# Performance work log

Measured on AMD Instinct MI355X. Metric: run time of the kernel, lower is better.

Reference implementation:

```python
import jax, jax.numpy as jnp
import numpy as np

B, N, FEAT = 64, 1024, 3
HID, STATE, LAYERS, NTYPES = 64, 32, 2, 10


def setup_inputs() -> dict:
    key = jax.random.key(0)
    ks = jax.random.split(key, 16)
    s = 0.1
    return {
        "task_features": jax.random.normal(ks[0], (B, N, FEAT), jnp.float32),
        "task_types": jax.random.randint(ks[1], (B, N), 0, NTYPES, jnp.int32),
        "prev_state": jnp.zeros((B, STATE), jnp.float32),
        "enc_w1": jax.random.normal(ks[2], (HID, FEAT), jnp.float32) * s,
        "enc_b1": jnp.zeros((HID,), jnp.float32),
        "enc_w2": jax.random.normal(ks[3], (HID, HID), jnp.float32) * s,
        "enc_b2": jnp.zeros((HID,), jnp.float32),
        "contention": jax.random.normal(ks[4], (NTYPES, NTYPES), jnp.float32) * 0.1,
        "gnn_w": jax.random.normal(ks[5], (LAYERS, HID, HID), jnp.float32) * s,
        "gnn_b": jnp.zeros((LAYERS, HID), jnp.float32),
        "gru_w_ih": jax.random.normal(ks[6], (3 * STATE, HID), jnp.float32) * s,
        "gru_w_hh": jax.random.normal(ks[7], (3 * STATE, STATE), jnp.float32) * s,
        "gru_b_ih": jnp.zeros((3 * STATE,), jnp.float32),
        "gru_b_hh": jnp.zeros((3 * STATE,), jnp.float32),
        "head_w1": jax.random.normal(ks[8], (HID, HID + STATE), jnp.float32) * s,
        "head_b1": jnp.zeros((HID,), jnp.float32),
        "head_w2": jax.random.normal(ks[9], (1, HID), jnp.float32) * s,
        "head_b2": jnp.zeros((1,), jnp.float32),
    }


def _forward(task_features, task_types, prev_state, enc_w1, enc_b1, enc_w2, enc_b2,
             contention, gnn_w, gnn_b, gru_w_ih, gru_w_hh, gru_b_ih, gru_b_hh,
             head_w1, head_b1, head_w2, head_b2):
    # task encoder: Linear -> ReLU -> Linear
    emb = jax.nn.relu(task_features @ enc_w1.T + enc_b1) @ enc_w2.T + enc_b2  # (B,N,H)
    # interaction graph: type-pair gather + cosine similarity
    base = contention[task_types[:, :, None], task_types[:, None, :]]  # (B,N,N)
    nrm = emb / jnp.maximum(jnp.linalg.norm(emb, axis=-1, keepdims=True), 1e-12)
    sim = jnp.einsum("bnd,bmd->bnm", nrm, nrm)
    adjacency = jax.nn.sigmoid(base) * sim  # (B,N,N)
    # GNN layers: aggregate + linear + relu
    h = emb
    for l in range(LAYERS):
        agg = jnp.einsum("bnm,bmd->bnd", adjacency, h)
        h = jax.nn.relu((h + agg) @ gnn_w[l].T + gnn_b[l])
    ctx = h.mean(axis=1)  # (B,H)
    # GRUCell (torch semantics)
    gi = ctx @ gru_w_ih.T + gru_b_ih
    gh = prev_state @ gru_w_hh.T + gru_b_hh
    i_r, i_z, i_n = jnp.split(gi, 3, axis=-1)
    h_r, h_z, h_n = jnp.split(gh, 3, axis=-1)
    r = jax.nn.sigmoid(i_r + h_r)
    z = jax.nn.sigmoid(i_z + h_z)
    n = jnp.tanh(i_n + r * h_n)
    new_state = (1.0 - z) * n + z * prev_state  # (B,S)
    # latency head on [h, state]
    st = jnp.broadcast_to(new_state[:, None, :], (h.shape[0], h.shape[1], new_state.shape[-1]))
    combined = jnp.concatenate([h, st], axis=-1)
    lat = jax.nn.relu(combined @ head_w1.T + head_b1) @ head_w2.T + head_b2
    return lat[..., 0], new_state


def reference(task_features, task_types, prev_state, enc_w1, enc_b1, enc_w2, enc_b2,
              contention, gnn_w, gnn_b, gru_w_ih, gru_w_hh, gru_b_ih, gru_b_hh,
              head_w1, head_b1, head_w2, head_b2):
    return _forward(task_features, task_types, prev_state, enc_w1, enc_b1, enc_w2, enc_b2,
                    contention, gnn_w, gnn_b, gru_w_ih, gru_w_hh, gru_b_ih, gru_b_hh,
                    head_w1, head_b1, head_w2, head_b2)
```

## Files before the change

### kernel.cpp

```cpp
#include <hip/hip_runtime.h>
#include <math.h>

#define BB 64
#define NN 1024
#define HID 64
#define STATE 32
#define NTYPES 10

typedef _Float16 f16;
typedef f16 f16x8 __attribute__((ext_vector_type(8)));
typedef float f32x4 __attribute__((ext_vector_type(4)));

#define MFMA16(a, b, c) __builtin_amdgcn_mfma_f32_16x16x32_f16(a, b, c, 0, 0, 0)

__device__ __forceinline__ float sigm(float x) { return 1.f / (1.f + expf(-x)); }

__device__ __forceinline__ f16x8 cvt8(float4 a, float4 b) {
    f16x8 r;
    r[0] = (f16)a.x; r[1] = (f16)a.y; r[2] = (f16)a.z; r[3] = (f16)a.w;
    r[4] = (f16)b.x; r[5] = (f16)b.y; r[6] = (f16)b.z; r[7] = (f16)b.w;
    return r;
}

__global__ __launch_bounds__(256) void k_prep(
    const float* __restrict__ w2, const float* __restrict__ gw,
    const float* __restrict__ hw1, f16* __restrict__ out)
{
    int p = blockIdx.x * 256 + threadIdx.x;
    if (p >= 18432) return;
    const float* W; int K, pl;
    if (p < 12288) { int seg = p >> 12; pl = p & 4095; W = (seg == 0) ? w2 : gw + (seg - 1) * 4096; K = 64; }
    else { W = hw1; K = 96; pl = p - 12288; }
    int j = pl & 7, lane = (pl >> 3) & 63, nt = (pl >> 9) & 3, ch = pl >> 11;
    int k = ch * 32 + ((lane >> 4) << 3) + j;
    int o = nt * 16 + (lane & 15);
    out[p] = (f16)W[o * K + k];
}

__global__ __launch_bounds__(256) void k_encoder(
    const float* __restrict__ feat,
    const float* __restrict__ w1, const float* __restrict__ b1,
    const f16* __restrict__ w2f, const float* __restrict__ b2,
    float* __restrict__ emb, float* __restrict__ nrm)
{
    __shared__ f16 w2s[4096];
    __shared__ f16 tmp[4][16 * 72];
    __shared__ float fbuf[4][48];
    int tid = threadIdx.x, wave = tid >> 6, lane = tid & 63;
    int l15 = lane & 15, quad = lane >> 4;
    { const uint4* s = (const uint4*)w2f; uint4* d = (uint4*)w2s;
      for (int i = tid; i < 512; i += 256) d[i] = s[i]; }
    float w10 = w1[lane * 3], w11 = w1[lane * 3 + 1], w12 = w1[lane * 3 + 2], b1l = b1[lane];
    int tb = blockIdx.x * 64 + wave * 16;
    if (lane < 48) fbuf[wave][lane] = feat[tb * 3 + lane];
    __syncthreads();
    f16* tw = &tmp[wave][0];
#pragma unroll
    for (int r = 0; r < 16; ++r) {
        float x0 = fbuf[wave][r * 3], x1 = fbuf[wave][r * 3 + 1], x2 = fbuf[wave][r * 3 + 2];
        float hv = fmaxf(fmaf(w10, x0, fmaf(w11, x1, fmaf(w12, x2, b1l))), 0.f);
        tw[r * 72 + lane] = (f16)hv;
    }
    __builtin_amdgcn_sched_barrier(0);
    f16x8 a0 = *(const f16x8*)&tw[l15 * 72 + quad * 8];
    f16x8 a1 = *(const f16x8*)&tw[l15 * 72 + 32 + quad * 8];
    const f16x8* bf = (const f16x8*)w2s;
    f32x4 acc[4];
#pragma unroll
    for (int nt = 0; nt < 4; ++nt) {
        f32x4 c = {0.f, 0.f, 0.f, 0.f};
        c = MFMA16(a0, bf[(0 * 4 + nt) * 64 + lane], c);
        c = MFMA16(a1, bf[(1 * 4 + nt) * 64 + lane], c);
        acc[nt] = c;
    }
    float b2c[4];
#pragma unroll
    for (int nt = 0; nt < 4; ++nt) b2c[nt] = b2[nt * 16 + l15];
#pragma unroll
    for (int i = 0; i < 4; ++i) {
        float v[4]; float ss = 0.f;
#pragma unroll
        for (int nt = 0; nt < 4; ++nt) { v[nt] = acc[nt][i] + b2c[nt]; ss = fmaf(v[nt], v[nt], ss); }
        ss += __shfl_xor(ss, 1, 64); ss += __shfl_xor(ss, 2, 64);
        ss += __shfl_xor(ss, 4, 64); ss += __shfl_xor(ss, 8, 64);
        float rinv = 1.f / fmaxf(sqrtf(ss), 1e-12f);
        int grow = tb + quad * 4 + i;
#pragma unroll
        for (int nt = 0; nt < 4; ++nt) {
            emb[grow * 64 + nt * 16 + l15] = v[nt];
            nrm[grow * 64 + nt * 16 + l15] = v[nt] * rinv;
        }
    }
}

__global__ __launch_bounds__(256) void k_bucket(
    const int* __restrict__ types, int* __restrict__ idx, int* __restrict__ cnt,
    float* __restrict__ ctx)
{
    int b = blockIdx.x;
    __shared__ int lcnt[NTYPES];
    if (threadIdx.x < NTYPES) lcnt[threadIdx.x] = 0;
    if (threadIdx.x < HID) ctx[b * HID + threadIdx.x] = 0.f;
    __syncthreads();
    for (int m = threadIdx.x; m < NN; m += 256) {
        int t = types[b * NN + m];
        int pos = atomicAdd(&lcnt[t], 1);
        idx[(b * NTYPES + t) * NN + pos] = m;
    }
    __syncthreads();
    if (threadIdx.x < NTYPES) cnt[b * NTYPES + threadIdx.x] = lcnt[threadIdx.x];
}

__global__ __launch_bounds__(256) void k_buildM(
    const int* __restrict__ idx, const int* __restrict__ cnt,
    const float* __restrict__ nrm, const float* __restrict__ h,
    f16* __restrict__ M)
{
    int b = blockIdx.x / NTYPES, j = blockIdx.x % NTYPES;
    int c = cnt[b * NTYPES + j];
    const int* lst = idx + (b * NTYPES + j) * NN;
    int kq = threadIdx.x >> 4, dq = threadIdx.x & 15;
    float acc[4][4] = {};
    const float4* nrm4 = (const float4*)(nrm + (size_t)b * NN * HID);
    const float4* h4   = (const float4*)(h   + (size_t)b * NN * HID);
    int e = 0;
    for (; e + 8 <= c; e += 8) {
        int ms[8];
#pragma unroll
        for (int u = 0; u < 8; ++u) ms[u] = lst[e + u];
        float4 av4[8], hv4[8];
#pragma unroll
        for (int u = 0; u < 8; ++u) { av4[u] = nrm4[ms[u] * 16 + kq]; hv4[u] = h4[ms[u] * 16 + dq]; }
#pragma unroll
        for (int u = 0; u < 8; ++u) {
            float av[4] = {av4[u].x, av4[u].y, av4[u].z, av4[u].w};
            float hv[4] = {hv4[u].x, hv4[u].y, hv4[u].z, hv4[u].w};
#pragma unroll
            for (int i = 0; i < 4; ++i)
#pragma unroll
                for (int q = 0; q < 4; ++q)
                    acc[i][q] = fmaf(av[i], hv[q], acc[i][q]);
        }
    }
    for (; e < c; ++e) {
        int m = lst[e];
        float4 a = nrm4[m * 16 + kq];
        float4 hh = h4[m * 16 + dq];
        float av[4] = {a.x, a.y, a.z, a.w};
        float hv[4] = {hh.x, hh.y, hh.z, hh.w};
#pragma unroll
        for (int i = 0; i < 4; ++i)
#pragma unroll
            for (int q = 0; q < 4; ++q)
                acc[i][q] = fmaf(av[i], hv[q], acc[i][q]);
    }
    f16* Mo = M + ((size_t)(b * NTYPES + j)) * HID * HID;
#pragma unroll
    for (int i = 0; i < 4; ++i) {
        union { f16 h[4]; uint2 u; } pk;
#pragma unroll
        for (int q = 0; q < 4; ++q) pk.h[q] = (f16)acc[i][q];
        *(uint2*)&Mo[(kq * 4 + i) * 64 + dq * 4] = pk.u;
    }
}

__global__ __launch_bounds__(256) void k_gnn_layer(
    const int* __restrict__ idx, const int* __restrict__ cnt,
    const float* __restrict__ cont, const f16* __restrict__ M,
    const float* __restrict__ nrm, const float* __restrict__ h,
    const f16* __restrict__ gwf, const float* __restrict__ gb,
    float* __restrict__ hout, float* __restrict__ ctx)
{
    __shared__ f16 cs[4096];
    __shared__ f16 gs[4096];
    __shared__ f16 tmp[4][16 * 72];
    int b = blockIdx.x / NTYPES, t = blockIdx.x % NTYPES;
    int c = cnt[b * NTYPES + t];
    if (c == 0) return;
    int tid = threadIdx.x, wave = tid >> 6, lane = tid & 63;
    int l15 = lane & 15, quad = lane >> 4;
    { const uint4* s2 = (const uint4*)gwf; uint4* d2 = (uint4*)gs;
      for (int i = tid; i < 512; i += 256) d2[i] = s2[i]; }
    {
        float sg[NTYPES];
#pragma unroll
        for (int j = 0; j < NTYPES; ++j) sg[j] = sigm(cont[t * NTYPES + j]);
        const f16* Mb = M + (size_t)b * NTYPES * 4096;
        for (int p = tid; p < 4096; p += 256) {
            float a = 0.f;
#pragma unroll
            for (int j = 0; j < NTYPES; ++j) a = fmaf(sg[j], (float)Mb[j * 4096 + p], a);
            int k = p >> 6, n = p & 63;
            int pos = (((k >> 5) * 4 + (n >> 4)) * 64 + ((k >> 3) & 3) * 16 + (n & 15)) * 8 + (k & 7);
            cs[pos] = (f16)a;
        }
    }
    float gbl[4];
#pragma unroll
    for (int nt = 0; nt < 4; ++nt) gbl[nt] = gb[nt * 16 + l15];
    const int* lst = idx + (b * NTYPES + t) * NN;
    const float* nb = nrm + (size_t)b * NN * HID;
    const float* hb = h + (size_t)b * NN * HID;
    float* hob = hout + (size_t)b * NN * HID;
    __syncthreads();
    const f16x8* cbf = (const f16x8*)cs;
    const f16x8* gbf = (const f16x8*)gs;
    f16* tw = &tmp[wave][0];
    float cacc[4] = {0.f, 0.f, 0.f, 0.f};
    for (int tb = wave * 16; tb < c; tb += 64) {
        int rA = tb + l15; if (rA >= c) rA = c - 1;
        int mA = lst[rA];
        const float4* na = (const float4*)(nb + (size_t)mA * 64);
        f16x8 a0 = cvt8(na[quad * 2], na[quad * 2 + 1]);
        f16x8 a1 = cvt8(na[8 + quad * 2], na[8 + quad * 2 + 1]);
        int rS[4], mS[4]; float hl[4][4];
#pragma unroll
        for (int i = 0; i < 4; ++i) {
            rS[i] = tb + quad * 4 + i;
            int rc = rS[i] < c ? rS[i] : c - 1;
            mS[i] = lst[rc];
#pragma unroll
            for (int nt = 0; nt < 4; ++nt) hl[nt][i] = hb[(size_t)mS[i] * 64 + nt * 16 + l15];
        }
        f32x4 acc[4];
#pragma unroll
        for (int nt = 0; nt < 4; ++nt) {
            f32x4 cc = {0.f, 0.f, 0.f, 0.f};
            cc = MFMA16(a0, cbf[(0 * 4 + nt) * 64 + lane], cc);
            cc = MFMA16(a1, cbf[(1 * 4 + nt) * 64 + lane], cc);
            acc[nt] = cc;
        }
#pragma unroll
        for (int nt = 0; nt < 4; ++nt)
#pragma unroll
            for (int i = 0; i < 4; ++i)
                tw[(quad * 4 + i) * 72 + nt * 16 + l15] = (f16)(acc[nt][i] + hl[nt][i]);
        __builtin_amdgcn_sched_barrier(0);
        f16x8 t0 = *(const f16x8*)&tw[l15 * 72 + quad * 8];
        f16x8 t1 = *(const f16x8*)&tw[l15 * 72 + 32 + quad * 8];
#pragma unroll
        for (int nt = 0; nt < 4; ++nt) {
            f32x4 o = {0.f, 0.f, 0.f, 0.f};
            o = MFMA16(t0, gbf[(0 * 4 + nt) * 64 + lane], o);
            o = MFMA16(t1, gbf[(1 * 4 + nt) * 64 + lane], o);
#pragma unroll
            for (int i = 0; i < 4; ++i)
                if (rS[i] < c) {
                    float v = fmaxf(o[i] + gbl[nt], 0.f);
                    hob[(size_t)mS[i] * 64 + nt * 16 + l15] = v;
                    cacc[nt] += v;
                }
        }
        __builtin_amdgcn_sched_barrier(0);
    }
    if (ctx) {
#pragma unroll
        for (int nt = 0; nt < 4; ++nt) {
            float s = cacc[nt];
            s += __shfl_xor(s, 16, 64);
            s += __shfl_xor(s, 32, 64);
            if (quad == 0) atomicAdd(&ctx[b * HID + nt * 16 + l15], s);
        }
    }
}

__global__ __launch_bounds__(128) void k_gru(
    const float* __restrict__ ctx_sum, const float* __restrict__ prev,
    const float* __restrict__ w_ih, const float* __restrict__ w_hh,
    const float* __restrict__ b_ih, const float* __restrict__ b_hh,
    float* __restrict__ state_out)
{
    int b = blockIdx.x;
    int tid = threadIdx.x;
    __shared__ float cs[HID], ps[STATE], gis[96], ghs[96];
    if (tid < HID) cs[tid] = ctx_sum[b * HID + tid] * (1.f / NN);
    if (tid >= HID && tid < HID + STATE) ps[tid - HID] = prev[b * STATE + tid - HID];
    __syncthreads();
    if (tid < 96) {
        float gi = b_ih[tid];
#pragma unroll 8
        for (int k = 0; k < HID; ++k) gi = fmaf(w_ih[tid * HID + k], cs[k], gi);
        float gh = b_hh[tid];
#pragma unroll
        for (int k = 0; k < STATE; ++k) gh = fmaf(w_hh[tid * STATE + k], ps[k], gh);
        gis[tid] = gi; ghs[tid] = gh;
    }
    __syncthreads();
    if (tid < STATE) {
        float r = sigm(gis[tid] + ghs[tid]);
        float z = sigm(gis[32 + tid] + ghs[32 + tid]);
        float nn = tanhf(gis[64 + tid] + r * ghs[64 + tid]);
        float pv = ps[tid];
        state_out[b * STATE + tid] = (1.f - z) * nn + z * pv;
    }
}

__global__ __launch_bounds__(256) void k_head(
    const float* __restrict__ h2, const float* __restrict__ state,
    const f16* __restrict__ hwf, const float* __restrict__ b1,
    const float* __restrict__ w2, const float* __restrict__ b2,
    float* __restrict__ lat)
{
    __shared__ f16 ws_[6144];
    int tid = threadIdx.x, wave = tid >> 6, lane = tid & 63;
    int l15 = lane & 15, quad = lane >> 4;
    int b = blockIdx.x >> 4;
    { const uint4* s = (const uint4*)hwf; uint4* d = (uint4*)ws_;
      for (int i = tid; i < 768; i += 256) d[i] = s[i]; }
    float b1c[4], w2c[4];
#pragma unroll
    for (int nt = 0; nt < 4; ++nt) { b1c[nt] = b1[nt * 16 + l15]; w2c[nt] = w2[nt * 16 + l15]; }
    float b2v = b2[0];
    __syncthreads();
    int tb = blockIdx.x * 64 + wave * 16;
    int grow = tb + l15;
    const float4* ha = (const float4*)(h2 + (size_t)grow * 64);
    f16x8 a0 = cvt8(ha[quad * 2], ha[quad * 2 + 1]);
    f16x8 a1 = cvt8(ha[8 + quad * 2], ha[8 + quad * 2 + 1]);
    const float4* sp = (const float4*)(state + b * STATE);
    f16x8 a2 = cvt8(sp[quad * 2], sp[quad * 2 + 1]);
    const f16x8* bf = (const f16x8*)ws_;
    f32x4 acc[4];
#pragma unroll
    for (int nt = 0; nt < 4; ++nt) {
        f32x4 cc = {0.f, 0.f, 0.f, 0.f};
        cc = MFMA16(a0, bf[(0 * 4 + nt) * 64 + lane], cc);
        cc = MFMA16(a1, bf[(1 * 4 + nt) * 64 + lane], cc);
        cc = MFMA16(a2, bf[(2 * 4 + nt) * 64 + lane], cc);
        acc[nt] = cc;
    }
#pragma unroll
    for (int i = 0; i < 4; ++i) {
        float s = 0.f;
#pragma unroll
        for (int nt = 0; nt < 4; ++nt) s = fmaf(fmaxf(acc[nt][i] + b1c[nt], 0.f), w2c[nt], s);
        s += __shfl_xor(s, 1, 64); s += __shfl_xor(s, 2, 64);
        s += __shfl_xor(s, 4, 64); s += __shfl_xor(s, 8, 64);
        if (l15 == 0) lat[tb + quad * 4 + i] = s + b2v;
    }
}

extern "C" void kernel_launch(void* const* d_in, const int* in_sizes, int n_in,
                              void* d_out, int out_size, void* d_ws, size_t ws_size,
                              hipStream_t stream) {
    const float* feat   = (const float*)d_in[0];
    const int*   types  = (const int*)d_in[1];
    const float* prev   = (const float*)d_in[2];
    const float* enc_w1 = (const float*)d_in[3];
    const float* enc_b1 = (const float*)d_in[4];
    const float* enc_w2 = (const float*)d_in[5];
    const float* enc_b2 = (const float*)d_in[6];
    const float* cont   = (const float*)d_in[7];
    const float* gnn_w  = (const float*)d_in[8];
    const float* gnn_b  = (const float*)d_in[9];
    const float* w_ih   = (const float*)d_in[10];
    const float* w_hh   = (const float*)d_in[11];
    const float* b_ih   = (const float*)d_in[12];
    const float* b_hh   = (const float*)d_in[13];
    const float* hw1    = (const float*)d_in[14];
    const float* hb1    = (const float*)d_in[15];
    const float* hw2    = (const float*)d_in[16];
    const float* hb2    = (const float*)d_in[17];
    float* out = (float*)d_out;

    float* ws  = (float*)d_ws;
    float* h0  = ws;
    float* h1  = ws + 4194304;
    float* nrm = ws + 8388608;
    int*   idx = (int*)(ws + 12582912);
    int*   cnt = idx + BB * NTYPES * NN;
    f16*   M    = (f16*)(ws + 12582912 + 656000);
    f16*   wfrag = (f16*)(ws + 12582912 + 656000 + 1310720);
    float* ctx  = ws + 12582912 + 656000 + 1310720 + 9216;
    f16*   w2f  = wfrag;
    f16*   gw0f = wfrag + 4096;
    f16*   gw1f = wfrag + 8192;
    f16*   hwf  = wfrag + 12288;

    k_prep<<<72, 256, 0, stream>>>(enc_w2, gnn_w, hw1, wfrag);
    k_encoder<<<BB * NN / 64, 256, 0, stream>>>(feat, enc_w1, enc_b1, w2f, enc_b2, h0, nrm);
    k_bucket<<<BB, 256, 0, stream>>>(types, idx, cnt, ctx);
    k_buildM<<<BB * NTYPES, 256, 0, stream>>>(idx, cnt, nrm, h0, M);
    k_gnn_layer<<<BB * NTYPES, 256, 0, stream>>>(idx, cnt, cont, M, nrm, h0, gw0f, gnn_b, h1, nullptr);
    k_buildM<<<BB * NTYPES, 256, 0, stream>>>(idx, cnt, nrm, h1, M);
    k_gnn_layer<<<BB * NTYPES, 256, 0, stream>>>(idx, cnt, cont, M, nrm, h1, gw1f, gnn_b + HID, h0, ctx);
    k_gru<<<BB, 128, 0, stream>>>(ctx, prev, w_ih, w_hh, b_ih, b_hh, out + BB * NN);
    k_head<<<BB * NN / 64, 256, 0, stream>>>(h0, out + BB * NN, hwf, hb1, hw2, hb2, out);
}
```

Baseline: 204.8 us.

## Precompute C·W per type, split buildM and GNN over four blocks, fuse bucketing

Folds the GNN weight into the per-type aggregation matrix, so a new kernel computes D = C·W once per (batch, type). The layer kernel then does a single accumulated MFMA chain (nrm·D + h·W) and no longer runs a second MFMA pass through shared memory. buildM and the GNN layer are split across four blocks each to raise parallelism. Bucketing moves into the encoder using global atomics, and zeroing moves into the prep kernel. This drops one launch but adds the buildCD launches and makes index order nondeterministic.

```diff
diff --git a/kernel.cpp b/kernel.cpp
--- a/kernel.cpp
+++ b/kernel.cpp
@@ -22,25 +22,32 @@
     return r;
 }
 
-__global__ __launch_bounds__(256) void k_prep(
+__global__ __launch_bounds__(256) void k_misc(
     const float* __restrict__ w2, const float* __restrict__ gw,
-    const float* __restrict__ hw1, f16* __restrict__ out)
+    const float* __restrict__ hw1, f16* __restrict__ out,
+    int* __restrict__ cnt, float* __restrict__ ctx)
 {
     int p = blockIdx.x * 256 + threadIdx.x;
-    if (p >= 18432) return;
-    const float* W; int K, pl;
-    if (p < 12288) { int seg = p >> 12; pl = p & 4095; W = (seg == 0) ? w2 : gw + (seg - 1) * 4096; K = 64; }
-    else { W = hw1; K = 96; pl = p - 12288; }
-    int j = pl & 7, lane = (pl >> 3) & 63, nt = (pl >> 9) & 3, ch = pl >> 11;
-    int k = ch * 32 + ((lane >> 4) << 3) + j;
-    int o = nt * 16 + (lane & 15);
-    out[p] = (f16)W[o * K + k];
+    if (p < 18432) {
+        const float* W; int K, pl;
+        if (p < 12288) { int seg = p >> 12; pl = p & 4095; W = (seg == 0) ? w2 : gw + (seg - 1) * 4096; K = 64; }
+        else { W = hw1; K = 96; pl = p - 12288; }
+        int j = pl & 7, lane = (pl >> 3) & 63, nt = (pl >> 9) & 3, ch = pl >> 11;
+        int k = ch * 32 + ((lane >> 4) << 3) + j;
+        int o = nt * 16 + (lane & 15);
+        out[p] = (f16)W[o * K + k];
+        return;
+    }
+    int q = p - 18432;
+    if (q < BB * NTYPES) cnt[q] = 0;
+    else if (q < BB * NTYPES + BB * HID) ctx[q - BB * NTYPES] = 0.f;
 }
 
 __global__ __launch_bounds__(256) void k_encoder(
     const float* __restrict__ feat,
     const float* __restrict__ w1, const float* __restrict__ b1,
     const f16* __restrict__ w2f, const float* __restrict__ b2,
+    const int* __restrict__ types, int* __restrict__ idx, int* __restrict__ cnt,
     float* __restrict__ emb, float* __restrict__ nrm)
 {
     __shared__ f16 w2s[4096];
@@ -48,6 +55,13 @@
     __shared__ float fbuf[4][48];
     int tid = threadIdx.x, wave = tid >> 6, lane = tid & 63;
     int l15 = lane & 15, quad = lane >> 4;
+    if (tid < 64) {
+        int row = blockIdx.x * 64 + tid;
+        int b = row >> 10;
+        int t = types[row];
+        int pos = atomicAdd(&cnt[b * NTYPES + t], 1);
+        idx[(b * NTYPES + t) * NN + pos] = row & (NN - 1);
+    }
     { const uint4* s = (const uint4*)w2f; uint4* d = (uint4*)w2s;
       for (int i = tid; i < 512; i += 256) d[i] = s[i]; }
     float w10 = w1[lane * 3], w11 = w1[lane * 3 + 1], w12 = w1[lane * 3 + 2], b1l = b1[lane];
@@ -93,108 +107,114 @@
     }
 }
 
-__global__ __launch_bounds__(256) void k_bucket(
-    const int* __restrict__ types, int* __restrict__ idx, int* __restrict__ cnt,
-    float* __restrict__ ctx)
-{
-    int b = blockIdx.x;
-    __shared__ int lcnt[NTYPES];
-    if (threadIdx.x < NTYPES) lcnt[threadIdx.x] = 0;
-    if (threadIdx.x < HID) ctx[b * HID + threadIdx.x] = 0.f;
-    __syncthreads();
-    for (int m = threadIdx.x; m < NN; m += 256) {
-        int t = types[b * NN + m];
-        int pos = atomicAdd(&lcnt[t], 1);
-        idx[(b * NTYPES + t) * NN + pos] = m;
-    }
-    __syncthreads();
-    if (threadIdx.x < NTYPES) cnt[b * NTYPES + threadIdx.x] = lcnt[threadIdx.x];
-}
-
 __global__ __launch_bounds__(256) void k_buildM(
     const int* __restrict__ idx, const int* __restrict__ cnt,
     const float* __restrict__ nrm, const float* __restrict__ h,
     f16* __restrict__ M)
 {
-    int b = blockIdx.x / NTYPES, j = blockIdx.x % NTYPES;
+    int blk = blockIdx.x;
+    int s = blk & 3, bj = blk >> 2;
+    int b = bj / NTYPES, j = bj % NTYPES;
     int c = cnt[b * NTYPES + j];
     const int* lst = idx + (b * NTYPES + j) * NN;
-    int kq = threadIdx.x >> 4, dq = threadIdx.x & 15;
-    float acc[4][4] = {};
-    const float4* nrm4 = (const float4*)(nrm + (size_t)b * NN * HID);
-    const float4* h4   = (const float4*)(h   + (size_t)b * NN * HID);
+    int d = s * 16 + (threadIdx.x >> 4);
+    int e4 = threadIdx.x & 15;
+    const float* nb = nrm + (size_t)b * NN * HID;
+    const float4* h4 = (const float4*)(h + (size_t)b * NN * HID);
+    float acc[4] = {0.f, 0.f, 0.f, 0.f};
     int e = 0;
     for (; e + 8 <= c; e += 8) {
         int ms[8];
 #pragma unroll
         for (int u = 0; u < 8; ++u) ms[u] = lst[e + u];
-        float4 av4[8], hv4[8];
-#pragma unroll
-        for (int u = 0; u < 8; ++u) { av4[u] = nrm4[ms[u] * 16 + kq]; hv4[u] = h4[ms[u] * 16 + dq]; }
+        float w[8]; float4 hh[8];
+#pragma unroll
+        for (int u = 0; u < 8; ++u) { w[u] = nb[ms[u] * 64 + d]; hh[u] = h4[ms[u] * 16 + e4]; }
 #pragma unroll
         for (int u = 0; u < 8; ++u) {
-            float av[4] = {av4[u].x, av4[u].y, av4[u].z, av4[u].w};
-            float hv[4] = {hv4[u].x, hv4[u].y, hv4[u].z, hv4[u].w};
-#pragma unroll
-            for (int i = 0; i < 4; ++i)
-#pragma unroll
-                for (int q = 0; q < 4; ++q)
-                    acc[i][q] = fmaf(av[i], hv[q], acc[i][q]);
+            acc[0] = fmaf(w[u], hh[u].x, acc[0]);
+            acc[1] = fmaf(w[u], hh[u].y, acc[1]);
+            acc[2] = fmaf(w[u], hh[u].z, acc[2]);
+            acc[3] = fmaf(w[u], hh[u].w, acc[3]);
         }
     }
     for (; e < c; ++e) {
         int m = lst[e];
-        float4 a = nrm4[m * 16 + kq];
-        float4 hh = h4[m * 16 + dq];
-        float av[4] = {a.x, a.y, a.z, a.w};
-        float hv[4] = {hh.x, hh.y, hh.z, hh.w};
-#pragma unroll
-        for (int i = 0; i < 4; ++i)
-#pragma unroll
-            for (int q = 0; q < 4; ++q)
-                acc[i][q] = fmaf(av[i], hv[q], acc[i][q]);
-    }
-    f16* Mo = M + ((size_t)(b * NTYPES + j)) * HID * HID;
-#pragma unroll
-    for (int i = 0; i < 4; ++i) {
-        union { f16 h[4]; uint2 u; } pk;
-#pragma unroll
-        for (int q = 0; q < 4; ++q) pk.h[q] = (f16)acc[i][q];
-        *(uint2*)&Mo[(kq * 4 + i) * 64 + dq * 4] = pk.u;
+        float w = nb[m * 64 + d];
+        float4 hh = h4[m * 16 + e4];
+        acc[0] = fmaf(w, hh.x, acc[0]);
+        acc[1] = fmaf(w, hh.y, acc[1]);
+        acc[2] = fmaf(w, hh.z, acc[2]);
+        acc[3] = fmaf(w, hh.w, acc[3]);
+    }
+    union { f16 hv[4]; uint2 u; } pk;
+#pragma unroll
+    for (int q = 0; q < 4; ++q) pk.hv[q] = (f16)acc[q];
+    f16* Mo = M + ((size_t)(b * NTYPES + j)) * 4096;
+    *(uint2*)&Mo[d * 64 + e4 * 4] = pk.u;
+}
+
+__global__ __launch_bounds__(256) void k_buildCD(
+    const float* __restrict__ cont, const f16* __restrict__ M,
+    const f16* __restrict__ gwf, f16* __restrict__ Dfrag)
+{
+    __shared__ float Cs[64][68];
+    __shared__ f16 gs[4096];
+    int b = blockIdx.x / NTYPES, t = blockIdx.x % NTYPES;
+    int tid = threadIdx.x, wave = tid >> 6, lane = tid & 63;
+    int l15 = lane & 15, quad = lane >> 4;
+    { const uint4* s2 = (const uint4*)gwf; uint4* d2 = (uint4*)gs;
+      for (int i = tid; i < 512; i += 256) d2[i] = s2[i]; }
+    float sg[NTYPES];
+#pragma unroll
+    for (int j = 0; j < NTYPES; ++j) sg[j] = sigm(cont[t * NTYPES + j]);
+    const f16* Mb = M + (size_t)b * NTYPES * 4096;
+    for (int p = tid; p < 4096; p += 256) {
+        float a = 0.f;
+#pragma unroll
+        for (int j = 0; j < NTYPES; ++j) a = fmaf(sg[j], (float)Mb[j * 4096 + p], a);
+        Cs[p >> 6][p & 63] = a;
+    }
+    __syncthreads();
+    const float4* rc4 = (const float4*)&Cs[wave * 16 + l15][0];
+    f16x8 a0 = cvt8(rc4[quad * 2], rc4[quad * 2 + 1]);
+    f16x8 a1 = cvt8(rc4[8 + quad * 2], rc4[8 + quad * 2 + 1]);
+    const f16x8* gbf = (const f16x8*)gs;
+    f16* Do = Dfrag + (size_t)(b * NTYPES + t) * 4096;
+#pragma unroll
+    for (int nt = 0; nt < 4; ++nt) {
+        f32x4 dd = {0.f, 0.f, 0.f, 0.f};
+        dd = MFMA16(a0, gbf[(0 * 4 + nt) * 64 + lane], dd);
+        dd = MFMA16(a1, gbf[(1 * 4 + nt) * 64 + lane], dd);
+#pragma unroll
+        for (int i = 0; i < 4; ++i) {
+            int d = wave * 16 + quad * 4 + i;
+            int pos = (((d >> 5) * 4 + nt) * 64 + ((d >> 3) & 3) * 16 + l15) * 8 + (d & 7);
+            Do[pos] = (f16)dd[i];
+        }
     }
 }
 
 __global__ __launch_bounds__(256) void k_gnn_layer(
     const int* __restrict__ idx, const int* __restrict__ cnt,
-    const float* __restrict__ cont, const f16* __restrict__ M,
+    const f16* __restrict__ Dfrag,
     const float* __restrict__ nrm, const float* __restrict__ h,
     const f16* __restrict__ gwf, const float* __restrict__ gb,
     float* __restrict__ hout, float* __restrict__ ctx)
 {
-    __shared__ f16 cs[4096];
+    __shared__ f16 ds[4096];
     __shared__ f16 gs[4096];
-    __shared__ f16 tmp[4][16 * 72];
-    int b = blockIdx.x / NTYPES, t = blockIdx.x % NTYPES;
+    int blk = blockIdx.x;
+    int s = blk & 3, bt = blk >> 2;
+    int b = bt / NTYPES, t = bt % NTYPES;
     int c = cnt[b * NTYPES + t];
     if (c == 0) return;
     int tid = threadIdx.x, wave = tid >> 6, lane = tid & 63;
     int l15 = lane & 15, quad = lane >> 4;
-    { const uint4* s2 = (const uint4*)gwf; uint4* d2 = (uint4*)gs;
-      for (int i = tid; i < 512; i += 256) d2[i] = s2[i]; }
-    {
-        float sg[NTYPES];
-#pragma unroll
-        for (int j = 0; j < NTYPES; ++j) sg[j] = sigm(cont[t * NTYPES + j]);
-        const f16* Mb = M + (size_t)b * NTYPES * 4096;
-        for (int p = tid; p < 4096; p += 256) {
-            float a = 0.f;
-#pragma unroll
-            for (int j = 0; j < NTYPES; ++j) a = fmaf(sg[j], (float)Mb[j * 4096 + p], a);
-            int k = p >> 6, n = p & 63;
-            int pos = (((k >> 5) * 4 + (n >> 4)) * 64 + ((k >> 3) & 3) * 16 + (n & 15)) * 8 + (k & 7);
-            cs[pos] = (f16)a;
-        }
-    }
+    { const uint4* s1 = (const uint4*)(Dfrag + (size_t)bt * 4096);
+      const uint4* s2 = (const uint4*)gwf;
+      uint4* d1 = (uint4*)ds; uint4* d2 = (uint4*)gs;
+      for (int i = tid; i < 512; i += 256) { d1[i] = s1[i]; d2[i] = s2[i]; } }
     float gbl[4];
 #pragma unroll
     for (int nt = 0; nt < 4; ++nt) gbl[nt] = gb[nt * 16 + l15];
@@ -203,63 +223,50 @@
     const float* hb = h + (size_t)b * NN * HID;
     float* hob = hout + (size_t)b * NN * HID;
     __syncthreads();
-    const f16x8* cbf = (const f16x8*)cs;
+    const f16x8* dbf = (const f16x8*)ds;
     const f16x8* gbf = (const f16x8*)gs;
-    f16* tw = &tmp[wave][0];
     float cacc[4] = {0.f, 0.f, 0.f, 0.f};
-    for (int tb = wave * 16; tb < c; tb += 64) {
+    for (int g = wave * 4 + s; g * 16 < c; g += 16) {
+        int tb = g * 16;
         int rA = tb + l15; if (rA >= c) rA = c - 1;
         int mA = lst[rA];
         const float4* na = (const float4*)(nb + (size_t)mA * 64);
+        const float4* ha = (const float4*)(hb + (size_t)mA * 64);
         f16x8 a0 = cvt8(na[quad * 2], na[quad * 2 + 1]);
         f16x8 a1 = cvt8(na[8 + quad * 2], na[8 + quad * 2 + 1]);
-        int rS[4], mS[4]; float hl[4][4];
-#pragma unroll
-        for (int i = 0; i < 4; ++i) {
-            rS[i] = tb + quad * 4 + i;
-            int rc = rS[i] < c ? rS[i] : c - 1;
-            mS[i] = lst[rc];
-#pragma unroll
-            for (int nt = 0; nt < 4; ++nt) hl[nt][i] = hb[(size_t)mS[i] * 64 + nt * 16 + l15];
-        }
+        f16x8 h0 = cvt8(ha[quad * 2], ha[quad * 2 + 1]);
+        f16x8 h1 = cvt8(ha[8 + quad * 2], ha[8 + quad * 2 + 1]);
         f32x4 acc[4];
 #pragma unroll
         for (int nt = 0; nt < 4; ++nt) {
             f32x4 cc = {0.f, 0.f, 0.f, 0.f};
-            cc = MFMA16(a0, cbf[(0 * 4 + nt) * 64 + lane], cc);
-            cc = MFMA16(a1, cbf[(1 * 4 + nt) * 64 + lane], cc);
+            cc = MFMA16(a0, dbf[(0 * 4 + nt) * 64 + lane], cc);
+            cc = MFMA16(a1, dbf[(1 * 4 + nt) * 64 + lane], cc);
+            cc = MFMA16(h0, gbf[(0 * 4 + nt) * 64 + lane], cc);
+            cc = MFMA16(h1, gbf[(1 * 4 + nt) * 64 + lane], cc);
             acc[nt] = cc;
         }
 #pragma unroll
-        for (int nt = 0; nt < 4; ++nt)
-#pragma unroll
-            for (int i = 0; i < 4; ++i)
-                tw[(quad * 4 + i) * 72 + nt * 16 + l15] = (f16)(acc[nt][i] + hl[nt][i]);
-        __builtin_amdgcn_sched_barrier(0);
-        f16x8 t0 = *(const f16x8*)&tw[l15 * 72 + quad * 8];
-        f16x8 t1 = *(const f16x8*)&tw[l15 * 72 + 32 + quad * 8];
-#pragma unroll
-        for (int nt = 0; nt < 4; ++nt) {
-            f32x4 o = {0.f, 0.f, 0.f, 0.f};
-            o = MFMA16(t0, gbf[(0 * 4 + nt) * 64 + lane], o);
-            o = MFMA16(t1, gbf[(1 * 4 + nt) * 64 + lane], o);
-#pragma unroll
-            for (int i = 0; i < 4; ++i)
-                if (rS[i] < c) {
-                    float v = fmaxf(o[i] + gbl[nt], 0.f);
-                    hob[(size_t)mS[i] * 64 + nt * 16 + l15] = v;
+        for (int i = 0; i < 4; ++i) {
+            int r = tb + quad * 4 + i;
+            if (r < c) {
+                int m = lst[r];
+#pragma unroll
+                for (int nt = 0; nt < 4; ++nt) {
+                    float v = fmaxf(acc[nt][i] + gbl[nt], 0.f);
+                    hob[(size_t)m * 64 + nt * 16 + l15] = v;
                     cacc[nt] += v;
                 }
-        }
-        __builtin_amdgcn_sched_barrier(0);
+            }
+        }
     }
     if (ctx) {
 #pragma unroll
         for (int nt = 0; nt < 4; ++nt) {
-            float s = cacc[nt];
-            s += __shfl_xor(s, 16, 64);
-            s += __shfl_xor(s, 32, 64);
-            if (quad == 0) atomicAdd(&ctx[b * HID + nt * 16 + l15], s);
+            float sv = cacc[nt];
+            sv += __shfl_xor(sv, 16, 64);
+            sv += __shfl_xor(sv, 32, 64);
+            if (quad == 0) atomicAdd(&ctx[b * HID + nt * 16 + l15], sv);
         }
     }
 }
@@ -369,21 +376,24 @@
     float* nrm = ws + 8388608;
     int*   idx = (int*)(ws + 12582912);
     int*   cnt = idx + BB * NTYPES * NN;
-    f16*   M    = (f16*)(ws + 12582912 + 656000);
-    f16*   wfrag = (f16*)(ws + 12582912 + 656000 + 1310720);
-    float* ctx  = ws + 12582912 + 656000 + 1310720 + 9216;
+    f16*   M     = (f16*)(ws + 12582912 + 656000);
+    f16*   Dfrag = (f16*)(ws + 12582912 + 656000 + 1310720);
+    f16*   wfrag = (f16*)(ws + 12582912 + 656000 + 2621440);
+    float* ctx   = ws + 12582912 + 656000 + 2621440 + 9216;
     f16*   w2f  = wfrag;
     f16*   gw0f = wfrag + 4096;
     f16*   gw1f = wfrag + 8192;
     f16*   hwf  = wfrag + 12288;
 
-    k_prep<<<72, 256, 0, stream>>>(enc_w2, gnn_w, hw1, wfrag);
-    k_encoder<<<BB * NN / 64, 256, 0, stream>>>(feat, enc_w1, enc_b1, w2f, enc_b2, h0, nrm);
-    k_bucket<<<BB, 256, 0, stream>>>(types, idx, cnt, ctx);
-    k_buildM<<<BB * NTYPES, 256, 0, stream>>>(idx, cnt, nrm, h0, M);
-    k_gnn_layer<<<BB * NTYPES, 256, 0, stream>>>(idx, cnt, cont, M, nrm, h0, gw0f, gnn_b, h1, nullptr);
-    k_buildM<<<BB * NTYPES, 256, 0, stream>>>(idx, cnt, nrm, h1, M);
-    k_gnn_layer<<<BB * NTYPES, 256, 0, stream>>>(idx, cnt, cont, M, nrm, h1, gw1f, gnn_b + HID, h0, ctx);
+    k_misc<<<91, 256, 0, stream>>>(enc_w2, gnn_w, hw1, wfrag, cnt, ctx);
+    k_encoder<<<BB * NN / 64, 256, 0, stream>>>(feat, enc_w1, enc_b1, w2f, enc_b2,
+                                                types, idx, cnt, h0, nrm);
+    k_buildM<<<BB * NTYPES * 4, 256, 0, stream>>>(idx, cnt, nrm, h0, M);
+    k_buildCD<<<BB * NTYPES, 256, 0, stream>>>(cont, M, gw0f, Dfrag);
+    k_gnn_layer<<<BB * NTYPES * 4, 256, 0, stream>>>(idx, cnt, Dfrag, nrm, h0, gw0f, gnn_b, h1, nullptr);
+    k_buildM<<<BB * NTYPES * 4, 256, 0, stream>>>(idx, cnt, nrm, h1, M);
+    k_buildCD<<<BB * NTYPES, 256, 0, stream>>>(cont, M, gw1f, Dfrag);
+    k_gnn_layer<<<BB * NTYPES * 4, 256, 0, stream>>>(idx, cnt, Dfrag, nrm, h1, gw1f, gnn_b + HID, h0, ctx);
     k_gru<<<BB, 128, 0, stream>>>(ctx, prev, w_ih, w_hh, b_ih, b_hh, out + BB * NN);
     k_head<<<BB * NN / 64, 256, 0, stream>>>(h0, out + BB * NN, hwf, hb1, hw2, hb2, out);
 }
```

Result: slower. 267.2 us (+30.5%).
